# Performance work log

Measured on AMD Instinct MI355X. Metric: run time of the kernel, lower is better.

The kernel has to match this reference:

```python
import jax, jax.numpy as jnp
import numpy as np

B, S, D, M = 8, 32, 256, 2048
TOPK = 8

def setup_inputs() -> dict:
    key = jax.random.key(0)
    ks = jax.random.split(key, 10)
    def lin(kw, fan_in, fan_out):
        # kaiming normal (linear): std = 1/sqrt(fan_in); stored as [in, out]
        return jax.random.normal(kw, (fan_in, fan_out), jnp.float32) / jnp.sqrt(fan_in)
    return {
        "x": jax.random.normal(ks[0], (B, S, D), jnp.float32),
        "memory": jax.random.normal(ks[1], (M, D), jnp.float32) * 0.02,
        "Wq": lin(ks[2], D, D), "bq": jnp.zeros((D,), jnp.float32),
        "Wk": lin(ks[3], D, D), "bk": jnp.zeros((D,), jnp.float32),
        "Wv": lin(ks[4], D, D), "bv": jnp.zeros((D,), jnp.float32),
        "Wg": lin(ks[5], 2 * D, D), "bg": jnp.zeros((D,), jnp.float32),
    }

def reference(x, memory, Wq, bq, Wk, bk, Wv, bv, Wg, bg):
    batch, seq_len, d = x.shape
    scale = jnp.sqrt(jnp.float32(d))
    mem0 = jnp.broadcast_to(memory[None], (batch,) + memory.shape)  # [B,M,D]
    b_idx = jnp.arange(batch)[:, None]

    def step(mem, xt):  # mem [B,M,D], xt [B,D]
        q = xt @ Wq + bq                      # [B,D]
        k = mem @ Wk + bk                     # [B,M,D]
        v = mem @ Wv + bv                     # [B,M,D]
        logits = jnp.einsum('bd,bmd->bm', q, k) / scale
        attn = jax.nn.softmax(logits, axis=-1)            # [B,M]
        out = jnp.einsum('bm,bmd->bd', attn, v)           # [B,D]
        g = jax.nn.sigmoid(jnp.concatenate([xt, out], axis=-1) @ Wg + bg)  # [B,D]
        _, top_idx = jax.lax.top_k(attn, TOPK)            # [B,TOPK]
        old = jnp.take_along_axis(mem, top_idx[:, :, None], axis=1)        # [B,TOPK,D]
        new = (1.0 - g)[:, None, :] * old + g[:, None, :] * xt[:, None, :]
        mem = mem.at[b_idx, top_idx].set(new)
        return mem, out

    _, outs = jax.lax.scan(step, mem0, jnp.swapaxes(x, 0, 1))  # outs [S,B,D]
    return jnp.swapaxes(outs, 0, 1)  # [B,S,D]
```

## Files before the change

### kernel.cpp

```cpp
#include <hip/hip_runtime.h>
#include <math.h>

constexpr int B_ = 8, S_ = 32, D_ = 256, M_ = 2048;
constexpr int N_ = S_ * B_;
constexpr int TK = 8;
constexpr int NSLOT = 256;
constexpr int TOPC = 256;
constexpr int NCAND = NSLOT + TOPC;
constexpr int KSPLIT = 4;

__global__ void k_transpose(const float* __restrict__ Wk, float* __restrict__ WkT) {
  __shared__ float tile[32][33];
  int bx = blockIdx.x & 7, by = blockIdx.x >> 3;
  int x0 = bx * 32, y0 = by * 32;
  int tx = threadIdx.x & 31, ty = threadIdx.x >> 5;
  for (int j = ty; j < 32; j += 8) tile[j][tx] = Wk[(y0 + j) * D_ + x0 + tx];
  __syncthreads();
  for (int j = ty; j < 32; j += 8) WkT[(x0 + j) * D_ + y0 + tx] = tile[tx][j];
}

__global__ __launch_bounds__(256) void k_qproj(
    const float* __restrict__ x, const float* __restrict__ Wq,
    const float* __restrict__ bq, const float* __restrict__ bk,
    const float* __restrict__ WkT, const float* __restrict__ Wg,
    float* __restrict__ qt, float* __restrict__ qbk, float* __restrict__ xgp) {
  int n = blockIdx.x, tid = threadIdx.x;
  int t = n / B_, b = n % B_;
  __shared__ float xr[D_], qsh[D_];
  __shared__ float red[4];
  xr[tid] = x[(b * S_ + t) * D_ + tid];
  __syncthreads();
  float accq = bq[tid], accg = 0.f;
#pragma unroll 8
  for (int i = 0; i < D_; ++i) {
    float xv = xr[i];
    accq = fmaf(xv, Wq[i * D_ + tid], accq);
    accg = fmaf(xv, Wg[i * D_ + tid], accg);
  }
  qsh[tid] = accq;
  xgp[n * D_ + tid] = accg;
  float p = accq * bk[tid];
  for (int off = 32; off > 0; off >>= 1) p += __shfl_down(p, off, 64);
  if ((tid & 63) == 0) red[tid >> 6] = p;
  __syncthreads();
  float acct = 0.f;
#pragma unroll 8
  for (int i = 0; i < D_; ++i) acct = fmaf(qsh[i], WkT[i * D_ + tid], acct);
  qt[n * D_ + tid] = acct;
  if (tid == 0) qbk[n] = red[0] + red[1] + red[2] + red[3];
}

__global__ __launch_bounds__(256) void k_L0(
    const float* __restrict__ qt, const float* __restrict__ mem,
    const float* __restrict__ qbk, float* __restrict__ L0) {
  __shared__ float qtT[64 * 64];
  __shared__ float mT[64 * 64];
  const int tid = threadIdx.x;
  const int m0 = blockIdx.x * 64, n0 = blockIdx.y * 64;
  const int r = tid & 63, c = tid >> 6;
  const int lane = tid & 63, wv = tid >> 6;
  const int tx = lane & 15, ty = lane >> 4;
  const int mg = tx * 4, ng = (wv * 4 + ty) * 4;
  float acc[4][4];
#pragma unroll
  for (int i = 0; i < 4; ++i)
#pragma unroll
    for (int j = 0; j < 4; ++j) acc[i][j] = 0.f;
  for (int kc = 0; kc < 4; ++kc) {
    __syncthreads();
#pragma unroll
    for (int it = 0; it < 4; ++it) {
      int kq = (c * 4 + it) * 4;
      float4 a = *(const float4*)&qt[(n0 + r) * D_ + kc * 64 + kq];
      qtT[(kq + 0) * 64 + r] = a.x; qtT[(kq + 1) * 64 + r] = a.y;
      qtT[(kq + 2) * 64 + r] = a.z; qtT[(kq + 3) * 64 + r] = a.w;
      float4 bm = *(const float4*)&mem[(m0 + r) * D_ + kc * 64 + kq];
      mT[(kq + 0) * 64 + r] = bm.x; mT[(kq + 1) * 64 + r] = bm.y;
      mT[(kq + 2) * 64 + r] = bm.z; mT[(kq + 3) * 64 + r] = bm.w;
    }
    __syncthreads();
#pragma unroll 4
    for (int k = 0; k < 64; ++k) {
      float4 av = *(const float4*)&qtT[k * 64 + ng];
      float4 bv4 = *(const float4*)&mT[k * 64 + mg];
      acc[0][0] = fmaf(av.x, bv4.x, acc[0][0]); acc[0][1] = fmaf(av.x, bv4.y, acc[0][1]);
      acc[0][2] = fmaf(av.x, bv4.z, acc[0][2]); acc[0][3] = fmaf(av.x, bv4.w, acc[0][3]);
      acc[1][0] = fmaf(av.y, bv4.x, acc[1][0]); acc[1][1] = fmaf(av.y, bv4.y, acc[1][1]);
      acc[1][2] = fmaf(av.y, bv4.z, acc[1][2]); acc[1][3] = fmaf(av.y, bv4.w, acc[1][3]);
      acc[2][0] = fmaf(av.z, bv4.x, acc[2][0]); acc[2][1] = fmaf(av.z, bv4.y, acc[2][1]);
      acc[2][2] = fmaf(av.z, bv4.z, acc[2][2]); acc[2][3] = fmaf(av.z, bv4.w, acc[2][3]);
      acc[3][0] = fmaf(av.w, bv4.x, acc[3][0]); acc[3][1] = fmaf(av.w, bv4.y, acc[3][1]);
      acc[3][2] = fmaf(av.w, bv4.z, acc[3][2]); acc[3][3] = fmaf(av.w, bv4.w, acc[3][3]);
    }
  }
#pragma unroll
  for (int i = 0; i < 4; ++i) {
    int n = n0 + ng + i;
    float qbv = qbk[n];
    float4 o;
    o.x = (acc[i][0] + qbv) * 0.0625f; o.y = (acc[i][1] + qbv) * 0.0625f;
    o.z = (acc[i][2] + qbv) * 0.0625f; o.w = (acc[i][3] + qbv) * 0.0625f;
    *(float4*)&L0[n * M_ + m0 + mg] = o;
  }
}

__global__ __launch_bounds__(256) void k_sortstats(const float* __restrict__ L0,
                                                   float* __restrict__ topv,
                                                   int* __restrict__ topi,
                                                   float* __restrict__ M0,
                                                   double* __restrict__ SumE0) {
  int n = blockIdx.x, tid = threadIdx.x;
  __shared__ float v[M_];
  __shared__ short ix[M_];
  __shared__ double redd[4];
  for (int m = tid; m < M_; m += 256) {
    v[m] = L0[(size_t)n * M_ + m];
    ix[m] = (short)m;
  }
  __syncthreads();
  for (int size = 2; size <= M_; size <<= 1) {
    for (int stride = size >> 1; stride > 0; stride >>= 1) {
      for (int i = tid; i < M_ / 2; i += 256) {
        int pos = 2 * i - (i & (stride - 1));
        int j = pos + stride;
        bool desc = ((pos & size) == 0);
        float va = v[pos], vb2 = v[j];
        short ia = ix[pos], ib = ix[j];
        bool aG = (va > vb2) || (va == vb2 && ia < ib);
        if (desc ? !aG : aG) { v[pos] = vb2; v[j] = va; ix[pos] = ib; ix[j] = ia; }
      }
      __syncthreads();
    }
  }
  topv[n * TOPC + tid] = v[tid];
  topi[n * TOPC + tid] = (int)ix[tid];
  float mx = v[0];
  if (tid == 0) M0[n] = mx;
  double s = 0.0;
  for (int m = tid; m < M_; m += 256) s += (double)expf(v[m] - mx);
  for (int off = 32; off > 0; off >>= 1) s += __shfl_down(s, off, 64);
  if ((tid & 63) == 0) redd[tid >> 6] = s;
  __syncthreads();
  if (tid == 0) SumE0[n] = redd[0] + redd[1] + redd[2] + redd[3];
}

__global__ __launch_bounds__(256) void k_ctxpart(
    const float* __restrict__ L0, const float* __restrict__ M0,
    const float* __restrict__ mem, float* __restrict__ ctxp) {
  int ks = blockIdx.x;
  int n0 = blockIdx.y * 32;
  int d0 = blockIdx.z * 64;
  int tid = threadIdx.x;
  __shared__ float Et[64 * 32];
  __shared__ float mTl[64 * 64];
  __shared__ float Msh[32];
  if (tid < 32) Msh[tid] = M0[n0 + tid];
  const int lane = tid & 63, wv = tid >> 6;
  const int tx = lane & 15, ty = lane >> 4;
  const int ng = (wv * 4 + ty) * 2;
  const int dg = tx * 4;
  float acc[2][4] = {{0, 0, 0, 0}, {0, 0, 0, 0}};
  for (int kc = 0; kc < 8; ++kc) {
    int kb = ks * 512 + kc * 64;
    __syncthreads();
#pragma unroll
    for (int j = 0; j < 8; ++j) {
      int ii = tid + 256 * j;
      int nr = ii & 31, kk = ii >> 5;
      Et[kk * 32 + nr] = expf(L0[(n0 + nr) * M_ + kb + kk] - Msh[nr]);
    }
    {
      int r = tid & 63, c = tid >> 6;
#pragma unroll
      for (int j = 0; j < 4; ++j) {
        int c4 = (c * 4 + j) * 4;
        *(float4*)&mTl[r * 64 + c4] = *(const float4*)&mem[(kb + r) * D_ + d0 + c4];
      }
    }
    __syncthreads();
#pragma unroll 4
    for (int kk = 0; kk < 64; ++kk) {
      float4 mv = *(const float4*)&mTl[kk * 64 + dg];
      float e0v = Et[kk * 32 + ng], e1v = Et[kk * 32 + ng + 1];
      acc[0][0] = fmaf(e0v, mv.x, acc[0][0]); acc[0][1] = fmaf(e0v, mv.y, acc[0][1]);
      acc[0][2] = fmaf(e0v, mv.z, acc[0][2]); acc[0][3] = fmaf(e0v, mv.w, acc[0][3]);
      acc[1][0] = fmaf(e1v, mv.x, acc[1][0]); acc[1][1] = fmaf(e1v, mv.y, acc[1][1]);
      acc[1][2] = fmaf(e1v, mv.z, acc[1][2]); acc[1][3] = fmaf(e1v, mv.w, acc[1][3]);
    }
  }
#pragma unroll
  for (int i = 0; i < 2; ++i) {
    int n = n0 + ng + i;
    *(float4*)&ctxp[((size_t)ks * N_ + n) * D_ + d0 + dg] =
        make_float4(acc[i][0], acc[i][1], acc[i][2], acc[i][3]);
  }
}

__global__ void k_ctxreduce(const float* __restrict__ ctxp, float* __restrict__ CTX0) {
  int idx = blockIdx.x * 256 + threadIdx.x;
  float s = 0.f;
#pragma unroll
  for (int ks = 0; ks < KSPLIT; ++ks) s += ctxp[(size_t)ks * N_ * D_ + idx];
  CTX0[idx] = s;
}

__global__ __launch_bounds__(256) void k_wvwg(const float* __restrict__ Wv,
                                              const float* __restrict__ Wg,
                                              const float* __restrict__ bv,
                                              const float* __restrict__ bg,
                                              float* __restrict__ WvWgB,
                                              float* __restrict__ bvg) {
  int blk = blockIdx.x;
  int tid = threadIdx.x;
  if (blk == 16) {
    float a = bg[tid];
#pragma unroll 8
    for (int j = 0; j < D_; ++j) a = fmaf(bv[j], Wg[(size_t)(D_ + j) * D_ + tid], a);
    bvg[tid] = a;
    return;
  }
  int i0 = (blk & 3) * 64, d0 = (blk >> 2) * 64;
  __shared__ float At[64 * 64];
  __shared__ float Bt[64 * 64];
  const int r = tid & 63, c = tid >> 6;
  const int lane = tid & 63, wvv = tid >> 6;
  const int tx = lane & 15, ty = lane >> 4;
  const int dg = tx * 4, ig = (wvv * 4 + ty) * 4;
  float acc[4][4];
#pragma unroll
  for (int i = 0; i < 4; ++i)
#pragma unroll
    for (int j = 0; j < 4; ++j) acc[i][j] = 0.f;
  for (int kc = 0; kc < 4; ++kc) {
    __syncthreads();
#pragma unroll
    for (int it = 0; it < 4; ++it) {
      int jq = (c * 4 + it) * 4;
      float4 a = *(const float4*)&Wv[(i0 + r) * D_ + kc * 64 + jq];
      At[(jq + 0) * 64 + r] = a.x; At[(jq + 1) * 64 + r] = a.y;
      At[(jq + 2) * 64 + r] = a.z; At[(jq + 3) * 64 + r] = a.w;
      int dq = (c * 4 + it) * 4;
      *(float4*)&Bt[r * 64 + dq] =
          *(const float4*)&Wg[(size_t)(D_ + kc * 64 + r) * D_ + d0 + dq];
    }
    __syncthreads();
#pragma unroll 4
    for (int j = 0; j < 64; ++j) {
      float4 av = *(const float4*)&At[j * 64 + ig];
      float4 bv4 = *(const float4*)&Bt[j * 64 + dg];
      acc[0][0] = fmaf(av.x, bv4.x, acc[0][0]); acc[0][1] = fmaf(av.x, bv4.y, acc[0][1]);
      acc[0][2] = fmaf(av.x, bv4.z, acc[0][2]); acc[0][3] = fmaf(av.x, bv4.w, acc[0][3]);
      acc[1][0] = fmaf(av.y, bv4.x, acc[1][0]); acc[1][1] = fmaf(av.y, bv4.y, acc[1][1]);
      acc[1][2] = fmaf(av.y, bv4.z, acc[1][2]); acc[1][3] = fmaf(av.y, bv4.w, acc[1][3]);
      acc[2][0] = fmaf(av.z, bv4.x, acc[2][0]); acc[2][1] = fmaf(av.z, bv4.y, acc[2][1]);
      acc[2][2] = fmaf(av.z, bv4.z, acc[2][2]); acc[2][3] = fmaf(av.z, bv4.w, acc[2][3]);
      acc[3][0] = fmaf(av.w, bv4.x, acc[3][0]); acc[3][1] = fmaf(av.w, bv4.y, acc[3][1]);
      acc[3][2] = fmaf(av.w, bv4.z, acc[3][2]); acc[3][3] = fmaf(av.w, bv4.w, acc[3][3]);
    }
  }
#pragma unroll
  for (int i = 0; i < 4; ++i) {
    *(float4*)&WvWgB[(size_t)(i0 + ig + i) * D_ + d0 + dg] =
        make_float4(acc[i][0], acc[i][1], acc[i][2], acc[i][3]);
  }
}

__global__ __launch_bounds__(1024, 1) void k_scan(
    const float* __restrict__ x, const float* __restrict__ mem0,
    const float* __restrict__ Wv, const float* __restrict__ bv,
    const float* __restrict__ WvWgB, const float* __restrict__ bvg,
    const float* __restrict__ qt, const float* __restrict__ qbk,
    const float* __restrict__ xgp, const float* __restrict__ L0,
    const float* __restrict__ M0, const double* __restrict__ SumE0,
    const float* __restrict__ CTX0, const float* __restrict__ topv,
    const int* __restrict__ topi, float* __restrict__ memcur,
    float* __restrict__ out) {
  const int b = blockIdx.x;
  const int tid = threadIdx.x;
  const int lane = tid & 63;
  const int wv = tid >> 6;

  __shared__ short tpos[M_];
  __shared__ int Tlist[NSLOT];
  __shared__ float curE[NSLOT], e0sA[NSLOT];
  __shared__ float candV[NCAND];
  __shared__ int candI[NCAND];
  __shared__ float dpart[15][D_];
  __shared__ float fpart[16][D_];
  __shared__ float qt_s[2][D_], xt_s[2][D_];
  __shared__ float g_s[D_];
  __shared__ float CTX0_s[D_], xgp_s[D_];
  __shared__ float bv_s[D_], bvg_s[D_];
  __shared__ float Msc[S_], qbks[S_];
  __shared__ double sum0s[S_];
  __shared__ float inv_esum;
  __shared__ int Tcount;
  __shared__ int selIdx[TK], selSlot[TK], selFresh[TK];

  for (int m = tid; m < M_; m += 1024) tpos[m] = -1;
  if (tid < S_) {
    Msc[tid] = M0[tid * B_ + b];
    qbks[tid] = qbk[tid * B_ + b];
  } else if (tid < 2 * S_) {
    sum0s[tid - S_] = SumE0[(tid - S_) * B_ + b];
  }
  if (tid >= 64 && tid < 64 + D_) {
    bv_s[tid - 64] = bv[tid - 64];
  } else if (tid < 64 + 2 * D_) {
    if (tid >= 64 + D_) bvg_s[tid - 64 - D_] = bvg[tid - 64 - D_];
  } else if (tid < 64 + 2 * D_ + 64) {
    int j = tid - (64 + 2 * D_);
    ((float4*)qt_s[0])[j] = ((const float4*)qt)[(size_t)b * 64 + j];
  } else if (tid < 64 + 2 * D_ + 128) {
    int j = tid - (64 + 2 * D_ + 64);
    ((float4*)xt_s[0])[j] = ((const float4*)x)[((size_t)b * S_) * 64 + j];
  }
  if (tid == 0) Tcount = 0;
  __syncthreads();

  for (int t = 0; t < S_; ++t) {
    const int n = t * B_ + b;
    const int par = t & 1;
    const int Tc = Tcount;
    const float c0 = Msc[t];
    const float qb = qbks[t];

    {
      int s = tid >> 2, part = tid & 3;
      float a = 0.f;
      if (s < Tc) {
        const float4* row = (const float4*)&memcur[((size_t)(b * NSLOT + s)) * D_] + part * 16;
        const float4* q4 = (const float4*)&qt_s[par][part * 64];
#pragma unroll
        for (int j = 0; j < 16; ++j) {
          float4 mv = row[j];
          float4 qv = q4[j];
          a = fmaf(mv.x, qv.x, a); a = fmaf(mv.y, qv.y, a);
          a = fmaf(mv.z, qv.z, a); a = fmaf(mv.w, qv.w, a);
        }
      }
      a += __shfl_xor(a, 1, 64);
      a += __shfl_xor(a, 2, 64);
      if (part == 0) {
        if (s < Tc) {
          float cur = (a + qb) * 0.0625f;
          int m = Tlist[s];
          curE[s] = expf(cur - c0);
          e0sA[s] = expf(L0[(size_t)n * M_ + m] - c0);
          candV[s] = cur;
          candI[s] = m;
        } else {
          candV[s] = -INFINITY;
          candI[s] = 0x7FFFFFFF;
        }
      } else if (part == 1) {
        int j = s;
        int ii = topi[n * TOPC + j];
        bool fresh = (tpos[ii] < 0);
        candV[NSLOT + j] = fresh ? topv[n * TOPC + j] : -INFINITY;
        candI[NSLOT + j] = fresh ? ii : 0x7FFFFFFF;
      } else if (part == 2) {
        if (s < 64) ((float4*)CTX0_s)[s] = ((const float4*)CTX0)[(size_t)n * 64 + s];
        else if (s < 128) ((float4*)xgp_s)[s - 64] = ((const float4*)xgp)[(size_t)n * 64 + (s - 64)];
      } else {
        if (t + 1 < S_) {
          if (s < 64)
            ((float4*)qt_s[par ^ 1])[s] = ((const float4*)qt)[(size_t)(n + B_) * 64 + s];
          else if (s < 128)
            ((float4*)xt_s[par ^ 1])[s - 64] =
                ((const float4*)x)[((size_t)b * S_ + t + 1) * 64 + (s - 64)];
        }
      }
    }
    __syncthreads();

    if (wv == 15) {
      float cv[8];
      int ci[8];
#pragma unroll
      for (int j = 0; j < 8; ++j) {
        cv[j] = candV[lane * 8 + j];
        ci[j] = candI[lane * 8 + j];
      }
      for (int r = 0; r < TK; ++r) {
        float bvv = cv[0];
        int bii = ci[0];
#pragma unroll
        for (int j = 1; j < 8; ++j)
          if (cv[j] > bvv || (cv[j] == bvv && ci[j] < bii)) { bvv = cv[j]; bii = ci[j]; }
#pragma unroll
        for (int off = 1; off < 64; off <<= 1) {
          float ov = __shfl_xor(bvv, off, 64);
          int oi = __shfl_xor(bii, off, 64);
          if (ov > bvv || (ov == bvv && oi < bii)) { bvv = ov; bii = oi; }
        }
        if (lane == 0) selIdx[r] = bii;
#pragma unroll
        for (int j = 0; j < 8; ++j)
          if (ci[j] == bii) { cv[j] = -INFINITY; ci[j] = 0x7FFFFFFF; }
      }
      if (lane == 0) {
        int tc = Tcount;
        for (int k = 0; k < TK; ++k) {
          int m = selIdx[k];
          int s = tpos[m];
          if (s < 0) {
            s = tc++;
            tpos[m] = (short)s;
            Tlist[s] = m;
            selFresh[k] = 1;
          } else
            selFresh[k] = 0;
          selSlot[k] = s;
        }
        Tcount = tc;
      }
      double ds = 0.0;
      for (int s = lane; s < Tc; s += 64) ds += (double)curE[s] - (double)e0sA[s];
      for (int off = 32; off > 0; off >>= 1) ds += __shfl_down(ds, off, 64);
      if (lane == 0) inv_esum = (float)(1.0 / (sum0s[t] + ds));
    } else {
      int d4 = lane, sp = wv;
      float4 acc = make_float4(0.f, 0.f, 0.f, 0.f);
      for (int s = sp; s < Tc; s += 15) {
        float e1 = curE[s], e0 = e0sA[s];
        int m = Tlist[s];
        float4 mc = ((const float4*)memcur)[((size_t)(b * NSLOT + s)) * 64 + d4];
        float4 mo = ((const float4*)mem0)[(size_t)m * 64 + d4];
        acc.x = fmaf(e1, mc.x, acc.x); acc.x = fmaf(-e0, mo.x, acc.x);
        acc.y = fmaf(e1, mc.y, acc.y); acc.y = fmaf(-e0, mo.y, acc.y);
        acc.z = fmaf(e1, mc.z, acc.z); acc.z = fmaf(-e0, mo.z, acc.z);
        acc.w = fmaf(e1, mc.w, acc.w); acc.w = fmaf(-e0, mo.w, acc.w);
      }
      ((float4*)dpart[sp])[d4] = acc;
    }
    __syncthreads();

    {
      int kp = wv & 7, k0 = kp * 32;
      float mynum = 0.f;
      if (lane < 32) {
        int k = k0 + lane;
        float nv = CTX0_s[k];
#pragma unroll
        for (int p = 0; p < 15; ++p) nv += dpart[p][k];
        mynum = nv;
      }
      const float4* Mp = (wv < 8) ? (const float4*)Wv : (const float4*)WvWgB;
      float4 acc = make_float4(0.f, 0.f, 0.f, 0.f);
#pragma unroll 8
      for (int i = 0; i < 32; ++i) {
        float nv = __shfl(mynum, i, 64);
        float4 w4 = Mp[(size_t)(k0 + i) * 64 + lane];
        acc.x = fmaf(nv, w4.x, acc.x); acc.y = fmaf(nv, w4.y, acc.y);
        acc.z = fmaf(nv, w4.z, acc.z); acc.w = fmaf(nv, w4.w, acc.w);
      }
      ((float4*)fpart[wv])[lane] = acc;
    }
    __syncthreads();

    if (tid < D_) {
      int d = tid;
      float o = 0.f;
#pragma unroll
      for (int p = 0; p < 8; ++p) o += fpart[p][d];
      o = o * inv_esum + bv_s[d];
      out[((size_t)b * S_ + t) * D_ + d] = o;
    } else if (tid < 2 * D_) {
      int d = tid - D_;
      float gg = 0.f;
#pragma unroll
      for (int p = 8; p < 16; ++p) gg += fpart[p][d];
      float gin = xgp_s[d] + gg * inv_esum + bvg_s[d];
      g_s[d] = 1.0f / (1.0f + expf(-gin));
    }
    __syncthreads();

    if (t < S_ - 1) {
      int d = tid & 255, part = tid >> 8;
#pragma unroll
      for (int kk = 0; kk < 2; ++kk) {
        int k = part * 2 + kk;
        int m = selIdx[k], s = selSlot[k];
        float oldv = selFresh[k] ? mem0[(size_t)m * D_ + d]
                                 : memcur[((size_t)(b * NSLOT + s)) * D_ + d];
        float gv = g_s[d];
        memcur[((size_t)(b * NSLOT + s)) * D_ + d] = (1.0f - gv) * oldv + gv * xt_s[par][d];
      }
      __syncthreads();
    }
  }
}

extern "C" void kernel_launch(void* const* d_in, const int* in_sizes, int n_in,
                              void* d_out, int out_size, void* d_ws, size_t ws_size,
                              hipStream_t stream) {
  const float* x = (const float*)d_in[0];
  const float* mem0 = (const float*)d_in[1];
  const float* Wq = (const float*)d_in[2];
  const float* bq = (const float*)d_in[3];
  const float* Wk = (const float*)d_in[4];
  const float* bk = (const float*)d_in[5];
  const float* Wv = (const float*)d_in[6];
  const float* bv = (const float*)d_in[7];
  const float* Wg = (const float*)d_in[8];
  const float* bg = (const float*)d_in[9];
  float* out = (float*)d_out;
  float* ws = (float*)d_ws;

  size_t o = 0;
  float* WkT = ws + o;   o += (size_t)D_ * D_;
  float* qt = ws + o;    o += (size_t)N_ * D_;
  float* qbk = ws + o;   o += N_;
  float* xgp = ws + o;   o += (size_t)N_ * D_;
  float* L0 = ws + o;    o += (size_t)N_ * M_;
  float* M0 = ws + o;    o += N_;
  double* SumE0 = (double*)(ws + o); o += 2 * N_;
  float* CTX0 = ws + o;  o += (size_t)N_ * D_;
  float* ctxp = ws + o;  o += (size_t)KSPLIT * N_ * D_;
  float* topv = ws + o;  o += (size_t)N_ * TOPC;
  int* topi = (int*)(ws + o); o += (size_t)N_ * TOPC;
  float* WvWgB = ws + o; o += (size_t)D_ * D_;
  float* bvg = ws + o;   o += D_;
  float* memcur = ws + o; o += (size_t)B_ * NSLOT * D_;

  k_transpose<<<dim3(64), dim3(256), 0, stream>>>(Wk, WkT);
  k_qproj<<<dim3(N_), dim3(256), 0, stream>>>(x, Wq, bq, bk, WkT, Wg, qt, qbk, xgp);
  k_L0<<<dim3(M_ / 64, N_ / 64), dim3(256), 0, stream>>>(qt, mem0, qbk, L0);
  k_sortstats<<<dim3(N_), dim3(256), 0, stream>>>(L0, topv, topi, M0, SumE0);
  k_ctxpart<<<dim3(KSPLIT, N_ / 32, D_ / 64), dim3(256), 0, stream>>>(L0, M0, mem0, ctxp);
  k_ctxreduce<<<dim3(N_), dim3(256), 0, stream>>>(ctxp, CTX0);
  k_wvwg<<<dim3(17), dim3(256), 0, stream>>>(Wv, Wg, bv, bg, WvWgB, bvg);
  k_scan<<<dim3(B_), dim3(1024), 0, stream>>>(x, mem0, Wv, bv, WvWgB, bvg, qt, qbk, xgp,
                                              L0, M0, SumE0, CTX0, topv, topi, memcur, out);
}
```

Measured before the change: 678.6 us.

## Track memory deltas and incremental slot-query dots inside scan, fuse prep kernels

New measurement: 937.0 us. 38.1% more time.

```diff
diff --git a/kernel.cpp b/kernel.cpp
--- a/kernel.cpp
+++ b/kernel.cpp
@@ -9,14 +9,76 @@
 constexpr int NCAND = NSLOT + TOPC;
 constexpr int KSPLIT = 4;
 
-__global__ void k_transpose(const float* __restrict__ Wk, float* __restrict__ WkT) {
-  __shared__ float tile[32][33];
-  int bx = blockIdx.x & 7, by = blockIdx.x >> 3;
-  int x0 = bx * 32, y0 = by * 32;
-  int tx = threadIdx.x & 31, ty = threadIdx.x >> 5;
-  for (int j = ty; j < 32; j += 8) tile[j][tx] = Wk[(y0 + j) * D_ + x0 + tx];
-  __syncthreads();
-  for (int j = ty; j < 32; j += 8) WkT[(x0 + j) * D_ + y0 + tx] = tile[tx][j];
+__global__ __launch_bounds__(256) void k_wvwgT(const float* __restrict__ Wv,
+                                               const float* __restrict__ Wg,
+                                               const float* __restrict__ bv,
+                                               const float* __restrict__ bg,
+                                               const float* __restrict__ Wk,
+                                               float* __restrict__ WvWgB,
+                                               float* __restrict__ bvg,
+                                               float* __restrict__ WkT) {
+  int blk = blockIdx.x;
+  int tid = threadIdx.x;
+  if (blk >= 17) {
+    __shared__ float tile[32][33];
+    int bb = blk - 17;
+    int bx = bb & 7, by = bb >> 3;
+    int x0 = bx * 32, y0 = by * 32;
+    int tx = tid & 31, ty = tid >> 5;
+    for (int j = ty; j < 32; j += 8) tile[j][tx] = Wk[(y0 + j) * D_ + x0 + tx];
+    __syncthreads();
+    for (int j = ty; j < 32; j += 8) WkT[(x0 + j) * D_ + y0 + tx] = tile[tx][j];
+    return;
+  }
+  if (blk == 16) {
+    float a = bg[tid];
+#pragma unroll 8
+    for (int j = 0; j < D_; ++j) a = fmaf(bv[j], Wg[(size_t)(D_ + j) * D_ + tid], a);
+    bvg[tid] = a;
+    return;
+  }
+  int i0 = (blk & 3) * 64, d0 = (blk >> 2) * 64;
+  __shared__ float At[64 * 64];
+  __shared__ float Bt[64 * 64];
+  const int r = tid & 63, c = tid >> 6;
+  const int lane = tid & 63, wvv = tid >> 6;
+  const int tx = lane & 15, ty = lane >> 4;
+  const int dg = tx * 4, ig = (wvv * 4 + ty) * 4;
+  float acc[4][4];
+#pragma unroll
+  for (int i = 0; i < 4; ++i)
+#pragma unroll
+    for (int j = 0; j < 4; ++j) acc[i][j] = 0.f;
+  for (int kc = 0; kc < 4; ++kc) {
+    __syncthreads();
+#pragma unroll
+    for (int it = 0; it < 4; ++it) {
+      int jq = (c * 4 + it) * 4;
+      float4 a = *(const float4*)&Wv[(i0 + r) * D_ + kc * 64 + jq];
+      At[(jq + 0) * 64 + r] = a.x; At[(jq + 1) * 64 + r] = a.y;
+      At[(jq + 2) * 64 + r] = a.z; At[(jq + 3) * 64 + r] = a.w;
+      *(float4*)&Bt[r * 64 + jq] =
+          *(const float4*)&Wg[(size_t)(D_ + kc * 64 + r) * D_ + d0 + jq];
+    }
+    __syncthreads();
+#pragma unroll 4
+    for (int j = 0; j < 64; ++j) {
+      float4 av = *(const float4*)&At[j * 64 + ig];
+      float4 bv4 = *(const float4*)&Bt[j * 64 + dg];
+      acc[0][0] = fmaf(av.x, bv4.x, acc[0][0]); acc[0][1] = fmaf(av.x, bv4.y, acc[0][1]);
+      acc[0][2] = fmaf(av.x, bv4.z, acc[0][2]); acc[0][3] = fmaf(av.x, bv4.w, acc[0][3]);
+      acc[1][0] = fmaf(av.y, bv4.x, acc[1][0]); acc[1][1] = fmaf(av.y, bv4.y, acc[1][1]);
+      acc[1][2] = fmaf(av.y, bv4.z, acc[1][2]); acc[1][3] = fmaf(av.y, bv4.w, acc[1][3]);
+      acc[2][0] = fmaf(av.z, bv4.x, acc[2][0]); acc[2][1] = fmaf(av.z, bv4.y, acc[2][1]);
+      acc[2][2] = fmaf(av.z, bv4.z, acc[2][2]); acc[2][3] = fmaf(av.z, bv4.w, acc[2][3]);
+      acc[3][0] = fmaf(av.w, bv4.x, acc[3][0]); acc[3][1] = fmaf(av.w, bv4.y, acc[3][1]);
+      acc[3][2] = fmaf(av.w, bv4.z, acc[3][2]); acc[3][3] = fmaf(av.w, bv4.w, acc[3][3]);
+    }
+  }
+#pragma unroll
+  for (int i = 0; i < 4; ++i)
+    *(float4*)&WvWgB[(size_t)(i0 + ig + i) * D_ + d0 + dg] =
+        make_float4(acc[i][0], acc[i][1], acc[i][2], acc[i][3]);
 }
 
 __global__ __launch_bounds__(256) void k_qproj(
@@ -196,75 +258,6 @@
   }
 }
 
-__global__ void k_ctxreduce(const float* __restrict__ ctxp, float* __restrict__ CTX0) {
-  int idx = blockIdx.x * 256 + threadIdx.x;
-  float s = 0.f;
-#pragma unroll
-  for (int ks = 0; ks < KSPLIT; ++ks) s += ctxp[(size_t)ks * N_ * D_ + idx];
-  CTX0[idx] = s;
-}
-
-__global__ __launch_bounds__(256) void k_wvwg(const float* __restrict__ Wv,
-                                              const float* __restrict__ Wg,
-                                              const float* __restrict__ bv,
-                                              const float* __restrict__ bg,
-                                              float* __restrict__ WvWgB,
-                                              float* __restrict__ bvg) {
-  int blk = blockIdx.x;
-  int tid = threadIdx.x;
-  if (blk == 16) {
-    float a = bg[tid];
-#pragma unroll 8
-    for (int j = 0; j < D_; ++j) a = fmaf(bv[j], Wg[(size_t)(D_ + j) * D_ + tid], a);
-    bvg[tid] = a;
-    return;
-  }
-  int i0 = (blk & 3) * 64, d0 = (blk >> 2) * 64;
-  __shared__ float At[64 * 64];
-  __shared__ float Bt[64 * 64];
-  const int r = tid & 63, c = tid >> 6;
-  const int lane = tid & 63, wvv = tid >> 6;
-  const int tx = lane & 15, ty = lane >> 4;
-  const int dg = tx * 4, ig = (wvv * 4 + ty) * 4;
-  float acc[4][4];
-#pragma unroll
-  for (int i = 0; i < 4; ++i)
-#pragma unroll
-    for (int j = 0; j < 4; ++j) acc[i][j] = 0.f;
-  for (int kc = 0; kc < 4; ++kc) {
-    __syncthreads();
-#pragma unroll
-    for (int it = 0; it < 4; ++it) {
-      int jq = (c * 4 + it) * 4;
-      float4 a = *(const float4*)&Wv[(i0 + r) * D_ + kc * 64 + jq];
-      At[(jq + 0) * 64 + r] = a.x; At[(jq + 1) * 64 + r] = a.y;
-      At[(jq + 2) * 64 + r] = a.z; At[(jq + 3) * 64 + r] = a.w;
-      int dq = (c * 4 + it) * 4;
-      *(float4*)&Bt[r * 64 + dq] =
-          *(const float4*)&Wg[(size_t)(D_ + kc * 64 + r) * D_ + d0 + dq];
-    }
-    __syncthreads();
-#pragma unroll 4
-    for (int j = 0; j < 64; ++j) {
-      float4 av = *(const float4*)&At[j * 64 + ig];
-      float4 bv4 = *(const float4*)&Bt[j * 64 + dg];
-      acc[0][0] = fmaf(av.x, bv4.x, acc[0][0]); acc[0][1] = fmaf(av.x, bv4.y, acc[0][1]);
-      acc[0][2] = fmaf(av.x, bv4.z, acc[0][2]); acc[0][3] = fmaf(av.x, bv4.w, acc[0][3]);
-      acc[1][0] = fmaf(av.y, bv4.x, acc[1][0]); acc[1][1] = fmaf(av.y, bv4.y, acc[1][1]);
-      acc[1][2] = fmaf(av.y, bv4.z, acc[1][2]); acc[1][3] = fmaf(av.y, bv4.w, acc[1][3]);
-      acc[2][0] = fmaf(av.z, bv4.x, acc[2][0]); acc[2][1] = fmaf(av.z, bv4.y, acc[2][1]);
-      acc[2][2] = fmaf(av.z, bv4.z, acc[2][2]); acc[2][3] = fmaf(av.z, bv4.w, acc[2][3]);
-      acc[3][0] = fmaf(av.w, bv4.x, acc[3][0]); acc[3][1] = fmaf(av.w, bv4.y, acc[3][1]);
-      acc[3][2] = fmaf(av.w, bv4.z, acc[3][2]); acc[3][3] = fmaf(av.w, bv4.w, acc[3][3]);
-    }
-  }
-#pragma unroll
-  for (int i = 0; i < 4; ++i) {
-    *(float4*)&WvWgB[(size_t)(i0 + ig + i) * D_ + d0 + dg] =
-        make_float4(acc[i][0], acc[i][1], acc[i][2], acc[i][3]);
-  }
-}
-
 __global__ __launch_bounds__(1024, 1) void k_scan(
     const float* __restrict__ x, const float* __restrict__ mem0,
     const float* __restrict__ Wv, const float* __restrict__ bv,
@@ -272,48 +265,62 @@
     const float* __restrict__ qt, const float* __restrict__ qbk,
     const float* __restrict__ xgp, const float* __restrict__ L0,
     const float* __restrict__ M0, const double* __restrict__ SumE0,
-    const float* __restrict__ CTX0, const float* __restrict__ topv,
-    const int* __restrict__ topi, float* __restrict__ memcur,
+    const float* __restrict__ ctxp, const float* __restrict__ topv,
+    const int* __restrict__ topi, float* __restrict__ U,
     float* __restrict__ out) {
   const int b = blockIdx.x;
   const int tid = threadIdx.x;
   const int lane = tid & 63;
-  const int wv = tid >> 6;
-
+  const int wvid = tid >> 6;
+
+  __shared__ float qtAll[S_][D_];
+  __shared__ float DOTS[S_][NSLOT];
+  __shared__ float utmp[TK][D_];
+  __shared__ float dpart[15][D_];
+  __shared__ float fpart[16][D_];
+  __shared__ float fpart2[16][D_];
   __shared__ short tpos[M_];
   __shared__ int Tlist[NSLOT];
   __shared__ float curE[NSLOT], e0sA[NSLOT];
   __shared__ float candV[NCAND];
   __shared__ int candI[NCAND];
-  __shared__ float dpart[15][D_];
-  __shared__ float fpart[16][D_];
-  __shared__ float qt_s[2][D_], xt_s[2][D_];
-  __shared__ float g_s[D_];
-  __shared__ float CTX0_s[D_], xgp_s[D_];
-  __shared__ float bv_s[D_], bvg_s[D_];
+  __shared__ float xt_s[2][D_];
+  __shared__ float CTX0_s[D_], xgp_s[D_], g_s[D_], bv_s[D_], bvg_s[D_];
   __shared__ float Msc[S_], qbks[S_];
   __shared__ double sum0s[S_];
   __shared__ float inv_esum;
   __shared__ int Tcount;
   __shared__ int selIdx[TK], selSlot[TK], selFresh[TK];
 
+  const float4* mem04 = (const float4*)mem0;
+  const float4* U4g = (const float4*)U;
+  const float4* Wv4 = (const float4*)Wv;
+  const float4* Wg4 = (const float4*)WvWgB;
+  const float4* qt4 = (const float4*)qt;
+  const float4* x4 = (const float4*)x;
+  const float4* ctxp4 = (const float4*)ctxp;
+  const float4* xgp4 = (const float4*)xgp;
+
+  float4 wreg[16];
+#pragma unroll
+  for (int j = 0; j < 16; ++j) wreg[j] = Wv4[(size_t)(wvid * 16 + j) * 64 + lane];
+
   for (int m = tid; m < M_; m += 1024) tpos[m] = -1;
+  for (int i = tid; i < S_ * 64; i += 1024) {
+    int tf = i >> 6, df = i & 63;
+    ((float4*)qtAll[tf])[df] = qt4[(size_t)(tf * B_ + b) * 64 + df];
+  }
   if (tid < S_) {
     Msc[tid] = M0[tid * B_ + b];
     qbks[tid] = qbk[tid * B_ + b];
-  } else if (tid < 2 * S_) {
-    sum0s[tid - S_] = SumE0[(tid - S_) * B_ + b];
-  }
-  if (tid >= 64 && tid < 64 + D_) {
-    bv_s[tid - 64] = bv[tid - 64];
-  } else if (tid < 64 + 2 * D_) {
-    if (tid >= 64 + D_) bvg_s[tid - 64 - D_] = bvg[tid - 64 - D_];
-  } else if (tid < 64 + 2 * D_ + 64) {
-    int j = tid - (64 + 2 * D_);
-    ((float4*)qt_s[0])[j] = ((const float4*)qt)[(size_t)b * 64 + j];
-  } else if (tid < 64 + 2 * D_ + 128) {
-    int j = tid - (64 + 2 * D_ + 64);
-    ((float4*)xt_s[0])[j] = ((const float4*)x)[((size_t)b * S_) * 64 + j];
+    sum0s[tid] = SumE0[tid * B_ + b];
+  } else if (tid >= 64 && tid < 64 + D_) {
+    int d = tid - 64;
+    bv_s[d] = bv[d];
+    bvg_s[d] = bvg[d];
+  } else if (tid >= 512 && tid < 576) {
+    int j = tid - 512;
+    ((float4*)xt_s[0])[j] = x4[(size_t)(b * S_) * 64 + j];
   }
   if (tid == 0) Tcount = 0;
   __syncthreads();
@@ -323,58 +330,49 @@
     const int par = t & 1;
     const int Tc = Tcount;
     const float c0 = Msc[t];
-    const float qb = qbks[t];
-
-    {
-      int s = tid >> 2, part = tid & 3;
-      float a = 0.f;
+
+    if (tid < NSLOT) {
+      int s = tid;
       if (s < Tc) {
-        const float4* row = (const float4*)&memcur[((size_t)(b * NSLOT + s)) * D_] + part * 16;
-        const float4* q4 = (const float4*)&qt_s[par][part * 64];
-#pragma unroll
-        for (int j = 0; j < 16; ++j) {
-          float4 mv = row[j];
-          float4 qv = q4[j];
-          a = fmaf(mv.x, qv.x, a); a = fmaf(mv.y, qv.y, a);
-          a = fmaf(mv.z, qv.z, a); a = fmaf(mv.w, qv.w, a);
-        }
-      }
-      a += __shfl_xor(a, 1, 64);
-      a += __shfl_xor(a, 2, 64);
-      if (part == 0) {
-        if (s < Tc) {
-          float cur = (a + qb) * 0.0625f;
-          int m = Tlist[s];
-          curE[s] = expf(cur - c0);
-          e0sA[s] = expf(L0[(size_t)n * M_ + m] - c0);
-          candV[s] = cur;
-          candI[s] = m;
-        } else {
-          candV[s] = -INFINITY;
-          candI[s] = 0x7FFFFFFF;
-        }
-      } else if (part == 1) {
-        int j = s;
-        int ii = topi[n * TOPC + j];
-        bool fresh = (tpos[ii] < 0);
-        candV[NSLOT + j] = fresh ? topv[n * TOPC + j] : -INFINITY;
-        candI[NSLOT + j] = fresh ? ii : 0x7FFFFFFF;
-      } else if (part == 2) {
-        if (s < 64) ((float4*)CTX0_s)[s] = ((const float4*)CTX0)[(size_t)n * 64 + s];
-        else if (s < 128) ((float4*)xgp_s)[s - 64] = ((const float4*)xgp)[(size_t)n * 64 + (s - 64)];
+        int m = Tlist[s];
+        float l0v = L0[(size_t)n * M_ + m];
+        float cur = l0v - DOTS[t][s] * 0.0625f;
+        curE[s] = expf(cur - c0);
+        e0sA[s] = expf(l0v - c0);
+        candV[s] = cur;
+        candI[s] = m;
       } else {
-        if (t + 1 < S_) {
-          if (s < 64)
-            ((float4*)qt_s[par ^ 1])[s] = ((const float4*)qt)[(size_t)(n + B_) * 64 + s];
-          else if (s < 128)
-            ((float4*)xt_s[par ^ 1])[s - 64] =
-                ((const float4*)x)[((size_t)b * S_ + t + 1) * 64 + (s - 64)];
-        }
-      }
-    }
-    __syncthreads();
-
-    if (wv == 15) {
+        candV[s] = -INFINITY;
+        candI[s] = 0x7FFFFFFF;
+      }
+    } else if (tid < 2 * NSLOT) {
+      int j = tid - NSLOT;
+      int ii = topi[n * TOPC + j];
+      bool fresh = (tpos[ii] < 0);
+      candV[NSLOT + j] = fresh ? topv[n * TOPC + j] : -INFINITY;
+      candI[NSLOT + j] = fresh ? ii : 0x7FFFFFFF;
+    } else if (tid < 512 + 64) {
+      int j = tid - 512;
+      float4 c0v = ctxp4[(size_t)(0 * N_ + n) * 64 + j];
+      float4 c1v = ctxp4[(size_t)(1 * N_ + n) * 64 + j];
+      float4 c2v = ctxp4[(size_t)(2 * N_ + n) * 64 + j];
+      float4 c3v = ctxp4[(size_t)(3 * N_ + n) * 64 + j];
+      ((float4*)CTX0_s)[j] = make_float4(c0v.x + c1v.x + c2v.x + c3v.x,
+                                         c0v.y + c1v.y + c2v.y + c3v.y,
+                                         c0v.z + c1v.z + c2v.z + c3v.z,
+                                         c0v.w + c1v.w + c2v.w + c3v.w);
+    } else if (tid < 512 + 128) {
+      int j = tid - (512 + 64);
+      ((float4*)xgp_s)[j] = xgp4[(size_t)n * 64 + j];
+    } else if (tid < 512 + 192) {
+      if (t + 1 < S_) {
+        int j = tid - (512 + 128);
+        ((float4*)xt_s[par ^ 1])[j] = x4[(size_t)(b * S_ + t + 1) * 64 + j];
+      }
+    }
+    __syncthreads();
+
+    if (wvid == 15) {
       float cv[8];
       int ci[8];
 #pragma unroll
@@ -420,42 +418,59 @@
       for (int off = 32; off > 0; off >>= 1) ds += __shfl_down(ds, off, 64);
       if (lane == 0) inv_esum = (float)(1.0 / (sum0s[t] + ds));
     } else {
-      int d4 = lane, sp = wv;
       float4 acc = make_float4(0.f, 0.f, 0.f, 0.f);
-      for (int s = sp; s < Tc; s += 15) {
-        float e1 = curE[s], e0 = e0sA[s];
-        int m = Tlist[s];
-        float4 mc = ((const float4*)memcur)[((size_t)(b * NSLOT + s)) * 64 + d4];
-        float4 mo = ((const float4*)mem0)[(size_t)m * 64 + d4];
-        acc.x = fmaf(e1, mc.x, acc.x); acc.x = fmaf(-e0, mo.x, acc.x);
-        acc.y = fmaf(e1, mc.y, acc.y); acc.y = fmaf(-e0, mo.y, acc.y);
-        acc.z = fmaf(e1, mc.z, acc.z); acc.z = fmaf(-e0, mo.z, acc.z);
-        acc.w = fmaf(e1, mc.w, acc.w); acc.w = fmaf(-e0, mo.w, acc.w);
-      }
-      ((float4*)dpart[sp])[d4] = acc;
+      int s = wvid;
+      float4 a_c, u_c;
+      if (s < Tc) {
+        a_c = mem04[(size_t)Tlist[s] * 64 + lane];
+        u_c = U4g[((size_t)(b * NSLOT + s)) * 64 + lane];
+      }
+      while (s < Tc) {
+        int s2 = s + 15;
+        float4 a_n, u_n;
+        if (s2 < Tc) {
+          a_n = mem04[(size_t)Tlist[s2] * 64 + lane];
+          u_n = U4g[((size_t)(b * NSLOT + s2)) * 64 + lane];
+        }
+        float ce = curE[s], w1 = ce - e0sA[s];
+        acc.x = fmaf(w1, a_c.x, acc.x); acc.x = fmaf(-ce, u_c.x, acc.x);
+        acc.y = fmaf(w1, a_c.y, acc.y); acc.y = fmaf(-ce, u_c.y, acc.y);
+        acc.z = fmaf(w1, a_c.z, acc.z); acc.z = fmaf(-ce, u_c.z, acc.z);
+        acc.w = fmaf(w1, a_c.w, acc.w); acc.w = fmaf(-ce, u_c.w, acc.w);
+        a_c = a_n;
+        u_c = u_n;
+        s = s2;
+      }
+      ((float4*)dpart[wvid])[lane] = acc;
     }
     __syncthreads();
 
     {
-      int kp = wv & 7, k0 = kp * 32;
       float mynum = 0.f;
-      if (lane < 32) {
-        int k = k0 + lane;
+      if (lane < 16) {
+        int k = wvid * 16 + lane;
         float nv = CTX0_s[k];
 #pragma unroll
         for (int p = 0; p < 15; ++p) nv += dpart[p][k];
         mynum = nv;
       }
-      const float4* Mp = (wv < 8) ? (const float4*)Wv : (const float4*)WvWgB;
       float4 acc = make_float4(0.f, 0.f, 0.f, 0.f);
+#pragma unroll
+      for (int j = 0; j < 16; ++j) {
+        float nv = __shfl(mynum, j, 64);
+        acc.x = fmaf(nv, wreg[j].x, acc.x); acc.y = fmaf(nv, wreg[j].y, acc.y);
+        acc.z = fmaf(nv, wreg[j].z, acc.z); acc.w = fmaf(nv, wreg[j].w, acc.w);
+      }
+      ((float4*)fpart[wvid])[lane] = acc;
+      float4 acc2 = make_float4(0.f, 0.f, 0.f, 0.f);
 #pragma unroll 8
-      for (int i = 0; i < 32; ++i) {
-        float nv = __shfl(mynum, i, 64);
-        float4 w4 = Mp[(size_t)(k0 + i) * 64 + lane];
-        acc.x = fmaf(nv, w4.x, acc.x); acc.y = fmaf(nv, w4.y, acc.y);
-        acc.z = fmaf(nv, w4.z, acc.z); acc.w = fmaf(nv, w4.w, acc.w);
-      }
-      ((float4*)fpart[wv])[lane] = acc;
+      for (int j = 0; j < 16; ++j) {
+        float nv = __shfl(mynum, j, 64);
+        float4 w4 = Wg4[(size_t)(wvid * 16 + j) * 64 + lane];
+        acc2.x = fmaf(nv, w4.x, acc2.x); acc2.y = fmaf(nv, w4.y, acc2.y);
+        acc2.z = fmaf(nv, w4.z, acc2.z); acc2.w = fmaf(nv, w4.w, acc2.w);
+      }
+      ((float4*)fpart2[wvid])[lane] = acc2;
     }
     __syncthreads();
 
@@ -463,29 +478,57 @@
       int d = tid;
       float o = 0.f;
 #pragma unroll
-      for (int p = 0; p < 8; ++p) o += fpart[p][d];
+      for (int p = 0; p < 16; ++p) o += fpart[p][d];
       o = o * inv_esum + bv_s[d];
       out[((size_t)b * S_ + t) * D_ + d] = o;
     } else if (tid < 2 * D_) {
       int d = tid - D_;
       float gg = 0.f;
 #pragma unroll
-      for (int p = 8; p < 16; ++p) gg += fpart[p][d];
+      for (int p = 0; p < 16; ++p) gg += fpart2[p][d];
       float gin = xgp_s[d] + gg * inv_esum + bvg_s[d];
       g_s[d] = 1.0f / (1.0f + expf(-gin));
     }
     __syncthreads();
 
     if (t < S_ - 1) {
-      int d = tid & 255, part = tid >> 8;
-#pragma unroll
-      for (int kk = 0; kk < 2; ++kk) {
-        int k = part * 2 + kk;
-        int m = selIdx[k], s = selSlot[k];
-        float oldv = selFresh[k] ? mem0[(size_t)m * D_ + d]
-                                 : memcur[((size_t)(b * NSLOT + s)) * D_ + d];
-        float gv = g_s[d];
-        memcur[((size_t)(b * NSLOT + s)) * D_ + d] = (1.0f - gv) * oldv + gv * xt_s[par][d];
+      {
+        int k = tid >> 7, dd = tid & 127;
+#pragma unroll
+        for (int h = 0; h < 2; ++h) {
+          int d = dd + h * 128;
+          int m = selIdx[k], s = selSlot[k];
+          float mo = mem0[(size_t)m * D_ + d];
+          float Uo = selFresh[k] ? 0.f : U[((size_t)(b * NSLOT + s)) * D_ + d];
+          float gv = g_s[d];
+          float u = gv * ((mo - Uo) - xt_s[par][d]);
+          U[((size_t)(b * NSLOT + s)) * D_ + d] = Uo + u;
+          utmp[k][d] = u;
+        }
+      }
+      __syncthreads();
+
+      {
+        int gid = tid >> 2, part = tid & 3;
+        int k = gid & 7, tf = t + 1 + (gid >> 3);
+        if (tf < S_) {
+          const float4* ut4 = (const float4*)utmp[k];
+          const float4* qa4 = (const float4*)qtAll[tf];
+          float a = 0.f;
+#pragma unroll
+          for (int j = 0; j < 16; ++j) {
+            float4 uv = ut4[j * 4 + part];
+            float4 qv = qa4[j * 4 + part];
+            a = fmaf(uv.x, qv.x, a); a = fmaf(uv.y, qv.y, a);
+            a = fmaf(uv.z, qv.z, a); a = fmaf(uv.w, qv.w, a);
+          }
+          a += __shfl_xor(a, 1, 64);
+          a += __shfl_xor(a, 2, 64);
+          if (part == 0) {
+            int s = selSlot[k];
+            DOTS[tf][s] = selFresh[k] ? a : (DOTS[tf][s] + a);
+          }
+        }
       }
       __syncthreads();
     }
@@ -516,21 +559,18 @@
   float* L0 = ws + o;    o += (size_t)N_ * M_;
   float* M0 = ws + o;    o += N_;
   double* SumE0 = (double*)(ws + o); o += 2 * N_;
-  float* CTX0 = ws + o;  o += (size_t)N_ * D_;
   float* ctxp = ws + o;  o += (size_t)KSPLIT * N_ * D_;
   float* topv = ws + o;  o += (size_t)N_ * TOPC;
   int* topi = (int*)(ws + o); o += (size_t)N_ * TOPC;
   float* WvWgB = ws + o; o += (size_t)D_ * D_;
   float* bvg = ws + o;   o += D_;
-  float* memcur = ws + o; o += (size_t)B_ * NSLOT * D_;
-
-  k_transpose<<<dim3(64), dim3(256), 0, stream>>>(Wk, WkT);
+  float* U = ws + o;     o += (size_t)B_ * NSLOT * D_;
+
+  k_wvwgT<<<dim3(81), dim3(256), 0, stream>>>(Wv, Wg, bv, bg, Wk, WvWgB, bvg, WkT);
   k_qproj<<<dim3(N_), dim3(256), 0, stream>>>(x, Wq, bq, bk, WkT, Wg, qt, qbk, xgp);
   k_L0<<<dim3(M_ / 64, N_ / 64), dim3(256), 0, stream>>>(qt, mem0, qbk, L0);
   k_sortstats<<<dim3(N_), dim3(256), 0, stream>>>(L0, topv, topi, M0, SumE0);
   k_ctxpart<<<dim3(KSPLIT, N_ / 32, D_ / 64), dim3(256), 0, stream>>>(L0, M0, mem0, ctxp);
-  k_ctxreduce<<<dim3(N_), dim3(256), 0, stream>>>(ctxp, CTX0);
-  k_wvwg<<<dim3(17), dim3(256), 0, stream>>>(Wv, Wg, bv, bg, WvWgB, bvg);
   k_scan<<<dim3(B_), dim3(1024), 0, stream>>>(x, mem0, Wv, bv, WvWgB, bvg, qt, qbk, xgp,
-                                              L0, M0, SumE0, CTX0, topv, topi, memcur, out);
-}
+                                              L0, M0, SumE0, ctxp, topv, topi, U, out);
+}
```
